# Performance work log

Hardware: AMD Instinct MI355X
Metric: run time of the kernel (lower is better)

## Reference

```python
import jax, jax.numpy as jnp
import numpy as np

N_HEAD = 16
MASK_VALUE = -10000.0


def setup_inputs() -> dict:
    key = jax.random.key(0)
    ks = jax.random.split(key, 5)
    B, S, D = 2, 2048, 1024
    return {
        "x": jax.random.normal(ks[0], (B, S, D), dtype=jnp.float32),
        "qkv_w": jax.random.normal(ks[1], (D, 3 * D), dtype=jnp.float32) * 0.02,
        "qkv_b": jnp.zeros((3 * D,), dtype=jnp.float32),
        "proj_w": jax.random.normal(ks[2], (D, D), dtype=jnp.float32) * 0.02,
        "proj_b": jnp.zeros((D,), dtype=jnp.float32),
    }


def reference(x, qkv_w, qkv_b, proj_w, proj_b):
    B, S, D = x.shape
    H = N_HEAD
    hd = D // H

    # fused QKV projection, then split (torch.split along last dim)
    qkv = x @ qkv_w + qkv_b                      # [B, S, 3D]
    q, k, v = jnp.split(qkv, 3, axis=-1)

    def split_heads(t):  # [B, S, D] -> [B, H, S, hd]
        return t.reshape(B, S, H, hd).transpose(0, 2, 1, 3)

    q, k, v = split_heads(q), split_heads(k), split_heads(v)

    # scaled dot-product scores (scale_attn_weights=True)
    scores = jnp.einsum("bhqd,bhkd->bhqk", q, k) / jnp.sqrt(jnp.asarray(hd, x.dtype))

    # causal mask: tril over [query_len, key_len] (no cache, so q_len == k_len == S)
    causal = jnp.tril(jnp.ones((S, S), dtype=bool))[None, None]
    scores = jnp.where(causal, scores, jnp.asarray(MASK_VALUE, x.dtype))

    attn = jax.nn.softmax(scores, axis=-1)       # dropout p=0 (eval): identity
    out = jnp.einsum("bhqk,bhkd->bhqd", attn, v)

    # merge heads and output projection (resid dropout p=0)
    out = out.transpose(0, 2, 1, 3).reshape(B, S, D)
    out = out @ proj_w + proj_b
    return out
```

## Files before the change

kernel.cpp:

```cpp
#include <hip/hip_runtime.h>
#include <hip/hip_bf16.h>


#define SEQ 2048
#define DM 1024
#define HD 64
#define NHEAD 16
#define BHTOT 32

typedef unsigned short u16;
typedef __bf16 bf16_t;
typedef bf16_t bf16x8 __attribute__((ext_vector_type(8)));
typedef float f32x4 __attribute__((ext_vector_type(4)));
typedef float f32x16 __attribute__((ext_vector_type(16)));

__device__ __forceinline__ u16 f2bf(float f) {
  unsigned u = __float_as_uint(f);
  u += 0x7fffu + ((u >> 16) & 1u);
  return (u16)(u >> 16);
}

__device__ __forceinline__ f32x4 mfma16(uint4 a, uint4 b, f32x4 c) {
  return __builtin_amdgcn_mfma_f32_16x16x32_bf16(
      __builtin_bit_cast(bf16x8, a), __builtin_bit_cast(bf16x8, b), c, 0, 0, 0);
}

__device__ __forceinline__ f32x16 mfma32(uint4 a, uint4 b, f32x16 c) {
  return __builtin_amdgcn_mfma_f32_32x32x16_bf16(
      __builtin_bit_cast(bf16x8, a), __builtin_bit_cast(bf16x8, b), c, 0, 0, 0);
}

__device__ __forceinline__ unsigned cvtpk(float lo, float hi) {
  unsigned d;
  asm("v_cvt_pk_bf16_f32 %0, %1, %2" : "=v"(d) : "v"(lo), "v"(hi));
  return d;
}

__device__ __forceinline__ void gload_lds16(const u16* g, void* l) {
  __builtin_amdgcn_global_load_lds(
      (const __attribute__((address_space(1))) unsigned*)g,
      (__attribute__((address_space(3))) unsigned*)l, 16, 0, 0);
}

__global__ __launch_bounds__(256) void cvt_bf16(const float* __restrict__ in,
                                                u16* __restrict__ out) {
  int i = (blockIdx.x * 256 + threadIdx.x) * 4;
  float4 v = *(const float4*)(in + i);
  uint2 pk;
  pk.x = (unsigned)f2bf(v.x) | ((unsigned)f2bf(v.y) << 16);
  pk.y = (unsigned)f2bf(v.z) | ((unsigned)f2bf(v.w) << 16);
  *(uint2*)(out + i) = pk;
}

__global__ __launch_bounds__(256) void transpose_w(const float* __restrict__ W,
                                                   u16* __restrict__ Wt,
                                                   int K, int N) {
  __shared__ u16 t[32][33];
  const int n0 = blockIdx.x * 32, k0 = blockIdx.y * 32;
  const int tx = threadIdx.x & 31, ty = threadIdx.x >> 5;
#pragma unroll
  for (int i = 0; i < 4; ++i) {
    int k = ty + i * 8;
    t[tx][k] = f2bf(W[(size_t)(k0 + k) * N + n0 + tx]);
  }
  __syncthreads();
#pragma unroll
  for (int i = 0; i < 4; ++i) {
    int n = ty + i * 8;
    Wt[(size_t)(n0 + n) * K + k0 + tx] = t[n][tx];
  }
}

__global__ __launch_bounds__(256) void qkv_gemm(
    const u16* __restrict__ A, const u16* __restrict__ Bt,
    const float* __restrict__ bias,
    u16* __restrict__ qb, u16* __restrict__ kb, u16* __restrict__ vb) {
  __shared__ u16 Al[128 * 32];
  __shared__ u16 Bl[128 * 32];
  const int tid = threadIdx.x;
  const int m0 = blockIdx.y * 128;
  const int n0 = blockIdx.x * 128;
  const int w = tid >> 6, lane = tid & 63;
  const int lr = lane & 15, lg = lane >> 4;
  const int wm = (w >> 1) * 64, wn = (w & 1) * 64;
  const int Kd = DM;

  f32x4 acc[4][4] = {};

  for (int kk = 0; kk < Kd; kk += 32) {
    __syncthreads();
#pragma unroll
    for (int i = 0; i < 2; ++i) {
      int off = (i * 4 + w) * 1024 + lane * 16;
      int row = off >> 6, colb = off & 63;
      gload_lds16(A + (size_t)(m0 + row) * Kd + kk + (colb >> 1),
                  (char*)Al + (i * 4 + w) * 1024);
      gload_lds16(Bt + (size_t)(n0 + row) * Kd + kk + (colb >> 1),
                  (char*)Bl + (i * 4 + w) * 1024);
    }
    __syncthreads();
    uint4 af[4], bfr[4];
#pragma unroll
    for (int mi = 0; mi < 4; ++mi)
      af[mi] = *(const uint4*)(Al + (wm + mi * 16 + lr) * 32 + lg * 8);
#pragma unroll
    for (int ni = 0; ni < 4; ++ni)
      bfr[ni] = *(const uint4*)(Bl + (wn + ni * 16 + lr) * 32 + lg * 8);
#pragma unroll
    for (int mi = 0; mi < 4; ++mi)
#pragma unroll
      for (int ni = 0; ni < 4; ++ni)
        acc[mi][ni] = mfma16(af[mi], bfr[ni], acc[mi][ni]);
  }

#pragma unroll
  for (int mi = 0; mi < 4; ++mi) {
#pragma unroll
    for (int ni = 0; ni < 4; ++ni) {
#pragma unroll
      for (int r = 0; r < 4; ++r) {
        int m = m0 + wm + mi * 16 + lg * 4 + r;
        int n = n0 + wn + ni * 16 + lr;
        float v = acc[mi][ni][r] + bias[n];
        int part = n >> 10;
        int d = n & 1023;
        int h = d >> 6, dim = d & 63;
        int b = m >> 11, s = m & 2047;
        int bh = b * NHEAD + h;
        if (part == 0)
          qb[((size_t)bh * SEQ + s) * HD + dim] = f2bf(v * 0.125f);
        else if (part == 1)
          kb[((size_t)bh * SEQ + s) * HD + dim] = f2bf(v);
        else
          vb[((size_t)bh * HD + dim) * SEQ + s] = f2bf(v);
      }
    }
  }
}

__global__ __launch_bounds__(256) void attn_kernel(
    const u16* __restrict__ Q, const u16* __restrict__ K,
    const u16* __restrict__ Vt, u16* __restrict__ O) {
  const int lane = threadIdx.x & 63;
  const int w = threadIdx.x >> 6;
  const int r31 = lane & 31;
  const int hi = lane >> 5;
  const int bh = blockIdx.x;
  const int y = blockIdx.y;
  const int qt = (w == 0) ? y : (w == 1) ? (31 - y) : (w == 2) ? (32 + y) : (63 - y);
  const int q0w = qt * 32;

  const u16* Qb = Q + (size_t)bh * SEQ * HD;
  const u16* Kb = K + (size_t)bh * SEQ * HD;
  const u16* Vb = Vt + (size_t)bh * HD * SEQ;

  uint4 qf[4];
#pragma unroll
  for (int ks = 0; ks < 4; ++ks)
    qf[ks] = *(const uint4*)(Qb + (size_t)(q0w + r31) * HD + ks * 16 + hi * 8);

  f32x16 ot0 = {}, ot1 = {};
  float M = -1e30f, L = 0.f;

  const int nst = (q0w >> 6) + 1;
  for (int t = 0; t < nst; ++t) {
    const int kv0 = t << 6;
    f32x16 s0 = {}, s1 = {};
#pragma unroll
    for (int ks = 0; ks < 4; ++ks) {
      uint4 kf0 = *(const uint4*)(Kb + (size_t)(kv0 + r31) * HD + ks * 16 + hi * 8);
      uint4 kf1 = *(const uint4*)(Kb + (size_t)(kv0 + 32 + r31) * HD + ks * 16 + hi * 8);
      s0 = mfma32(kf0, qf[ks], s0);
      s1 = mfma32(kf1, qf[ks], s1);
    }
    if (t == nst - 1) {
      const int q_abs = q0w + r31;
#pragma unroll
      for (int i = 0; i < 16; ++i) {
        int row = (i & 3) + 8 * (i >> 2) + 4 * hi;
        if (kv0 + row > q_abs) s0[i] = -1e30f;
        if (kv0 + 32 + row > q_abs) s1[i] = -1e30f;
      }
    }
    float pm = s0[0];
#pragma unroll
    for (int i = 1; i < 16; ++i) pm = fmaxf(pm, s0[i]);
#pragma unroll
    for (int i = 0; i < 16; ++i) pm = fmaxf(pm, s1[i]);
    pm = fmaxf(pm, __shfl_xor(pm, 32));
    const float newM = fmaxf(M, pm);
    const float sc = __expf(M - newM);
    M = newM;
    float rs = 0.f;
#pragma unroll
    for (int i = 0; i < 16; ++i) { s0[i] = __expf(s0[i] - newM); rs += s0[i]; }
#pragma unroll
    for (int i = 0; i < 16; ++i) { s1[i] = __expf(s1[i] - newM); rs += s1[i]; }
    rs += __shfl_xor(rs, 32);
    L = L * sc + rs;
#pragma unroll
    for (int i = 0; i < 16; ++i) { ot0[i] *= sc; ot1[i] *= sc; }

    uint4 pa[4];
#define RELAYOUT(dst, v0, v1, v2, v3, v4, v5, v6, v7)                    \
    {                                                                    \
      unsigned e01 = cvtpk(v0, v1), e23 = cvtpk(v2, v3);                 \
      unsigned e45 = cvtpk(v4, v5), e67 = cvtpk(v6, v7);                 \
      unsigned p01 = __shfl_xor(e01, 32), p23 = __shfl_xor(e23, 32);     \
      unsigned p45 = __shfl_xor(e45, 32), p67 = __shfl_xor(e67, 32);     \
      dst.x = hi ? p45 : e01;                                            \
      dst.y = hi ? p67 : e23;                                            \
      dst.z = hi ? e45 : p01;                                            \
      dst.w = hi ? e67 : p23;                                            \
    }
    RELAYOUT(pa[0], s0[0], s0[1], s0[2], s0[3], s0[4], s0[5], s0[6], s0[7]);
    RELAYOUT(pa[1], s0[8], s0[9], s0[10], s0[11], s0[12], s0[13], s0[14], s0[15]);
    RELAYOUT(pa[2], s1[0], s1[1], s1[2], s1[3], s1[4], s1[5], s1[6], s1[7]);
    RELAYOUT(pa[3], s1[8], s1[9], s1[10], s1[11], s1[12], s1[13], s1[14], s1[15]);
#undef RELAYOUT

#pragma unroll
    for (int ks = 0; ks < 4; ++ks) {
      uint4 vf0 = *(const uint4*)(Vb + (size_t)r31 * SEQ + kv0 + ks * 16 + hi * 8);
      uint4 vf1 = *(const uint4*)(Vb + (size_t)(32 + r31) * SEQ + kv0 + ks * 16 + hi * 8);
      ot0 = mfma32(vf0, pa[ks], ot0);
      ot1 = mfma32(vf1, pa[ks], ot1);
    }
  }

  const float inv = 1.0f / L;
  const int b = bh >> 4, h = bh & 15;
  u16* Orow = O + ((size_t)b * SEQ + q0w + r31) * DM + h * HD;
#pragma unroll
  for (int g = 0; g < 4; ++g) {
    uint2 p0, p1;
    p0.x = (unsigned)f2bf(ot0[4 * g + 0] * inv) | ((unsigned)f2bf(ot0[4 * g + 1] * inv) << 16);
    p0.y = (unsigned)f2bf(ot0[4 * g + 2] * inv) | ((unsigned)f2bf(ot0[4 * g + 3] * inv) << 16);
    p1.x = (unsigned)f2bf(ot1[4 * g + 0] * inv) | ((unsigned)f2bf(ot1[4 * g + 1] * inv) << 16);
    p1.y = (unsigned)f2bf(ot1[4 * g + 2] * inv) | ((unsigned)f2bf(ot1[4 * g + 3] * inv) << 16);
    *(uint2*)(Orow + 8 * g + 4 * hi) = p0;
    *(uint2*)(Orow + 32 + 8 * g + 4 * hi) = p1;
  }
}

__global__ __launch_bounds__(256) void proj_gemm(
    const u16* __restrict__ A, const u16* __restrict__ Bt,
    const float* __restrict__ bias, float* __restrict__ out) {
  __shared__ u16 Al[128 * 32];
  __shared__ u16 Bl[128 * 32];
  const int tid = threadIdx.x;
  const int m0 = blockIdx.y * 128;
  const int n0 = blockIdx.x * 128;
  const int w = tid >> 6, lane = tid & 63;
  const int lr = lane & 15, lg = lane >> 4;
  const int wm = (w >> 1) * 64, wn = (w & 1) * 64;
  const int Kd = DM;

  f32x4 acc[4][4] = {};

  for (int kk = 0; kk < Kd; kk += 32) {
    __syncthreads();
#pragma unroll
    for (int i = 0; i < 2; ++i) {
      int off = (i * 4 + w) * 1024 + lane * 16;
      int row = off >> 6, colb = off & 63;
      gload_lds16(A + (size_t)(m0 + row) * Kd + kk + (colb >> 1),
                  (char*)Al + (i * 4 + w) * 1024);
      gload_lds16(Bt + (size_t)(n0 + row) * Kd + kk + (colb >> 1),
                  (char*)Bl + (i * 4 + w) * 1024);
    }
    __syncthreads();
    uint4 af[4], bfr[4];
#pragma unroll
    for (int mi = 0; mi < 4; ++mi)
      af[mi] = *(const uint4*)(Al + (wm + mi * 16 + lr) * 32 + lg * 8);
#pragma unroll
    for (int ni = 0; ni < 4; ++ni)
      bfr[ni] = *(const uint4*)(Bl + (wn + ni * 16 + lr) * 32 + lg * 8);
#pragma unroll
    for (int mi = 0; mi < 4; ++mi)
#pragma unroll
      for (int ni = 0; ni < 4; ++ni)
        acc[mi][ni] = mfma16(af[mi], bfr[ni], acc[mi][ni]);
  }

#pragma unroll
  for (int mi = 0; mi < 4; ++mi)
#pragma unroll
    for (int ni = 0; ni < 4; ++ni)
#pragma unroll
      for (int r = 0; r < 4; ++r) {
        int m = m0 + wm + mi * 16 + lg * 4 + r;
        int n = n0 + wn + ni * 16 + lr;
        out[(size_t)m * DM + n] = acc[mi][ni][r] + bias[n];
      }
}

extern "C" void kernel_launch(void* const* d_in, const int* in_sizes, int n_in,
                              void* d_out, int out_size, void* d_ws, size_t ws_size,
                              hipStream_t stream) {
  const float* x      = (const float*)d_in[0];
  const float* qkv_w  = (const float*)d_in[1];
  const float* qkv_b  = (const float*)d_in[2];
  const float* proj_w = (const float*)d_in[3];
  const float* proj_b = (const float*)d_in[4];
  float* out = (float*)d_out;

  const size_t per = (size_t)BHTOT * SEQ * HD;
  u16* qb = (u16*)d_ws;
  u16* kb = qb + per;
  u16* vb = kb + per;
  u16* xb = vb + per;
  u16* ab = xb;
  u16* wqkvT = xb + (size_t)SEQ * 2 * DM;
  u16* wprojT = wqkvT + (size_t)DM * 3 * DM / 1;

  wprojT = wqkvT + (size_t)3072 * DM;

  dim3 blk(256);
  cvt_bf16<<<dim3(4096), blk, 0, stream>>>(x, xb);
  transpose_w<<<dim3(96, 32), blk, 0, stream>>>(qkv_w, wqkvT, DM, 3072);
  transpose_w<<<dim3(32, 32), blk, 0, stream>>>(proj_w, wprojT, DM, DM);
  qkv_gemm<<<dim3(24, 32), blk, 0, stream>>>(xb, wqkvT, qkv_b, qb, kb, vb);
  attn_kernel<<<dim3(BHTOT, 16), blk, 0, stream>>>(qb, kb, vb, ab);
  proj_gemm<<<dim3(8, 32), blk, 0, stream>>>(ab, wprojT, proj_b, out);
}
```

Measured before the change: 161.9 us.

## Restructure attention: paired q-tiles per block, K prefetch, exp2, lazy rescale, mask skip

Attention blocks now use 2 waves that handle adjacent 32-row query tiles sharing one KV step range, launched heaviest-first over a 1D grid of 1024 blocks. K tiles are double-buffered in registers so the next step's K load overlaps the current softmax and PV work. Q is prescaled by log2(e)/8 so exp2 can replace exp, and the running max is only rescaled when it grows by more than 8 (lazy rescaling). On the diagonal step, the fully masked half-tile is skipped for even query tiles. The trade-off is more register pressure from the double buffers, and lazy rescaling lets values grow up to 2^8 before renormalising.

Result: faster. 148.0 us (-8.6%).

```diff
diff --git a/kernel.cpp b/kernel.cpp
--- a/kernel.cpp
+++ b/kernel.cpp
@@ -128,7 +128,7 @@
         int b = m >> 11, s = m & 2047;
         int bh = b * NHEAD + h;
         if (part == 0)
-          qb[((size_t)bh * SEQ + s) * HD + dim] = f2bf(v * 0.125f);
+          qb[((size_t)bh * SEQ + s) * HD + dim] = f2bf(v * 0.18033688f);
         else if (part == 1)
           kb[((size_t)bh * SEQ + s) * HD + dim] = f2bf(v);
         else
@@ -138,17 +138,18 @@
   }
 }
 
-__global__ __launch_bounds__(256) void attn_kernel(
+__global__ __launch_bounds__(128) void attn_kernel(
     const u16* __restrict__ Q, const u16* __restrict__ K,
     const u16* __restrict__ Vt, u16* __restrict__ O) {
   const int lane = threadIdx.x & 63;
   const int w = threadIdx.x >> 6;
   const int r31 = lane & 31;
   const int hi = lane >> 5;
-  const int bh = blockIdx.x;
-  const int y = blockIdx.y;
-  const int qt = (w == 0) ? y : (w == 1) ? (31 - y) : (w == 2) ? (32 + y) : (63 - y);
+  const int bh = blockIdx.x & 31;
+  const int j = 31 - (blockIdx.x >> 5);
+  const int qt = 2 * j + w;
   const int q0w = qt * 32;
+  const int nst = j + 1;
 
   const u16* Qb = Q + (size_t)bh * SEQ * HD;
   const u16* Kb = K + (size_t)bh * SEQ * HD;
@@ -162,71 +163,123 @@
   f32x16 ot0 = {}, ot1 = {};
   float M = -1e30f, L = 0.f;
 
-  const int nst = (q0w >> 6) + 1;
-  for (int t = 0; t < nst; ++t) {
-    const int kv0 = t << 6;
-    f32x16 s0 = {}, s1 = {};
-#pragma unroll
-    for (int ks = 0; ks < 4; ++ks) {
-      uint4 kf0 = *(const uint4*)(Kb + (size_t)(kv0 + r31) * HD + ks * 16 + hi * 8);
-      uint4 kf1 = *(const uint4*)(Kb + (size_t)(kv0 + 32 + r31) * HD + ks * 16 + hi * 8);
-      s0 = mfma32(kf0, qf[ks], s0);
-      s1 = mfma32(kf1, qf[ks], s1);
-    }
-    if (t == nst - 1) {
-      const int q_abs = q0w + r31;
-#pragma unroll
-      for (int i = 0; i < 16; ++i) {
-        int row = (i & 3) + 8 * (i >> 2) + 4 * hi;
-        if (kv0 + row > q_abs) s0[i] = -1e30f;
-        if (kv0 + 32 + row > q_abs) s1[i] = -1e30f;
-      }
-    }
-    float pm = s0[0];
-#pragma unroll
-    for (int i = 1; i < 16; ++i) pm = fmaxf(pm, s0[i]);
-#pragma unroll
-    for (int i = 0; i < 16; ++i) pm = fmaxf(pm, s1[i]);
-    pm = fmaxf(pm, __shfl_xor(pm, 32));
-    const float newM = fmaxf(M, pm);
-    const float sc = __expf(M - newM);
-    M = newM;
-    float rs = 0.f;
-#pragma unroll
-    for (int i = 0; i < 16; ++i) { s0[i] = __expf(s0[i] - newM); rs += s0[i]; }
-#pragma unroll
-    for (int i = 0; i < 16; ++i) { s1[i] = __expf(s1[i] - newM); rs += s1[i]; }
-    rs += __shfl_xor(rs, 32);
-    L = L * sc + rs;
-#pragma unroll
-    for (int i = 0; i < 16; ++i) { ot0[i] *= sc; ot1[i] *= sc; }
-
-    uint4 pa[4];
-#define RELAYOUT(dst, v0, v1, v2, v3, v4, v5, v6, v7)                    \
-    {                                                                    \
-      unsigned e01 = cvtpk(v0, v1), e23 = cvtpk(v2, v3);                 \
-      unsigned e45 = cvtpk(v4, v5), e67 = cvtpk(v6, v7);                 \
-      unsigned p01 = __shfl_xor(e01, 32), p23 = __shfl_xor(e23, 32);     \
-      unsigned p45 = __shfl_xor(e45, 32), p67 = __shfl_xor(e67, 32);     \
-      dst.x = hi ? p45 : e01;                                            \
-      dst.y = hi ? p67 : e23;                                            \
-      dst.z = hi ? e45 : p01;                                            \
-      dst.w = hi ? e67 : p23;                                            \
-    }
-    RELAYOUT(pa[0], s0[0], s0[1], s0[2], s0[3], s0[4], s0[5], s0[6], s0[7]);
-    RELAYOUT(pa[1], s0[8], s0[9], s0[10], s0[11], s0[12], s0[13], s0[14], s0[15]);
-    RELAYOUT(pa[2], s1[0], s1[1], s1[2], s1[3], s1[4], s1[5], s1[6], s1[7]);
-    RELAYOUT(pa[3], s1[8], s1[9], s1[10], s1[11], s1[12], s1[13], s1[14], s1[15]);
+#define LOADK(KF, kv0)                                                          \
+  {                                                                             \
+    _Pragma("unroll") for (int ks = 0; ks < 4; ++ks) {                          \
+      KF[ks] = *(const uint4*)(Kb + (size_t)((kv0) + r31) * HD + ks * 16 + hi * 8); \
+      KF[ks + 4] =                                                              \
+          *(const uint4*)(Kb + (size_t)((kv0) + 32 + r31) * HD + ks * 16 + hi * 8); \
+    }                                                                           \
+  }
+
+#define RELAYOUT(dst, S, base)                                                  \
+  {                                                                             \
+    unsigned e01 = cvtpk(S[base + 0], S[base + 1]), e23 = cvtpk(S[base + 2], S[base + 3]); \
+    unsigned e45 = cvtpk(S[base + 4], S[base + 5]), e67 = cvtpk(S[base + 6], S[base + 7]); \
+    unsigned p01 = __shfl_xor(e01, 32), p23 = __shfl_xor(e23, 32);              \
+    unsigned p45 = __shfl_xor(e45, 32), p67 = __shfl_xor(e67, 32);              \
+    dst.x = hi ? p45 : e01;                                                     \
+    dst.y = hi ? p67 : e23;                                                     \
+    dst.z = hi ? e45 : p01;                                                     \
+    dst.w = hi ? e67 : p23;                                                     \
+  }
+
+#define STEP(KF, KN)                                                            \
+  {                                                                             \
+    const int kv0 = t << 6;                                                     \
+    const bool last = (t == nst - 1);                                           \
+    const bool skip1 = last && ((qt & 1) == 0);   \
+    uint4 vf[8];                                                                \
+    _Pragma("unroll") for (int ks = 0; ks < 2; ++ks) {                          \
+      vf[ks] = *(const uint4*)(Vb + (size_t)r31 * SEQ + kv0 + ks * 16 + hi * 8); \
+      vf[ks + 4] =                                                              \
+          *(const uint4*)(Vb + (size_t)(32 + r31) * SEQ + kv0 + ks * 16 + hi * 8); \
+    }                                                                           \
+    if (!skip1) {                                                               \
+      _Pragma("unroll") for (int ks = 2; ks < 4; ++ks) {                        \
+        vf[ks] = *(const uint4*)(Vb + (size_t)r31 * SEQ + kv0 + ks * 16 + hi * 8); \
+        vf[ks + 4] =                                                            \
+            *(const uint4*)(Vb + (size_t)(32 + r31) * SEQ + kv0 + ks * 16 + hi * 8); \
+      }                                                                         \
+    }                                                                           \
+    f32x16 s0 = {}, s1 = {};                                                    \
+    _Pragma("unroll") for (int ks = 0; ks < 4; ++ks)                            \
+        s0 = mfma32(KF[ks], qf[ks], s0);                                        \
+    if (!skip1) {                                                               \
+      _Pragma("unroll") for (int ks = 0; ks < 4; ++ks)                          \
+          s1 = mfma32(KF[ks + 4], qf[ks], s1);                                  \
+    }                                                                           \
+    if (t + 1 < nst) LOADK(KN, kv0 + 64);                                       \
+    if (last) {                                                                 \
+      _Pragma("unroll") for (int i = 0; i < 16; ++i) {                          \
+        const int row = (i & 3) + 8 * (i >> 2) + 4 * hi;                        \
+        if (skip1) {                                                            \
+          if (row > r31) s0[i] = -1e30f;                                        \
+        } else {                                                                \
+          if (row > r31) s1[i] = -1e30f;                                        \
+        }                                                                       \
+      }                                                                         \
+    }                                                                           \
+    float pm = s0[0];                                                           \
+    _Pragma("unroll") for (int i = 1; i < 16; ++i) pm = fmaxf(pm, s0[i]);       \
+    if (!skip1) {                                                               \
+      _Pragma("unroll") for (int i = 0; i < 16; ++i) pm = fmaxf(pm, s1[i]);     \
+    }                                                                           \
+    pm = fmaxf(pm, __shfl_xor(pm, 32));                                         \
+    if (!__all(pm - M <= 8.0f)) {   \
+      const float newM = fmaxf(M, pm);                                          \
+      const float sc = __builtin_exp2f(M - newM);                               \
+      M = newM;                                                                 \
+      L *= sc;                                                                  \
+      _Pragma("unroll") for (int i = 0; i < 16; ++i) {                          \
+        ot0[i] *= sc;                                                           \
+        ot1[i] *= sc;                                                           \
+      }                                                                         \
+    }                                                                           \
+    float rs = 0.f;                                                             \
+    _Pragma("unroll") for (int i = 0; i < 16; ++i) {                            \
+      s0[i] = __builtin_exp2f(s0[i] - M);                                       \
+      rs += s0[i];                                                              \
+    }                                                                           \
+    if (!skip1) {                                                               \
+      _Pragma("unroll") for (int i = 0; i < 16; ++i) {                          \
+        s1[i] = __builtin_exp2f(s1[i] - M);                                     \
+        rs += s1[i];                                                            \
+      }                                                                         \
+    }                                                                           \
+    rs += __shfl_xor(rs, 32);                                                   \
+    L += rs;                                                                    \
+    uint4 pa[4];                                                                \
+    RELAYOUT(pa[0], s0, 0);                                                     \
+    RELAYOUT(pa[1], s0, 8);                                                     \
+    if (!skip1) {                                                               \
+      RELAYOUT(pa[2], s1, 0);                                                   \
+      RELAYOUT(pa[3], s1, 8);                                                   \
+    }                                                                           \
+    _Pragma("unroll") for (int ks = 0; ks < 2; ++ks) {                          \
+      ot0 = mfma32(vf[ks], pa[ks], ot0);                                        \
+      ot1 = mfma32(vf[ks + 4], pa[ks], ot1);                                    \
+    }                                                                           \
+    if (!skip1) {                                                               \
+      _Pragma("unroll") for (int ks = 2; ks < 4; ++ks) {                        \
+        ot0 = mfma32(vf[ks], pa[ks], ot0);                                      \
+        ot1 = mfma32(vf[ks + 4], pa[ks], ot1);                                  \
+      }                                                                         \
+    }                                                                           \
+  }
+
+  uint4 kA[8], kB[8];
+  LOADK(kA, 0);
+  int t = 0;
+  for (;;) {
+    STEP(kA, kB);
+    if (++t >= nst) break;
+    STEP(kB, kA);
+    if (++t >= nst) break;
+  }
+#undef STEP
 #undef RELAYOUT
-
-#pragma unroll
-    for (int ks = 0; ks < 4; ++ks) {
-      uint4 vf0 = *(const uint4*)(Vb + (size_t)r31 * SEQ + kv0 + ks * 16 + hi * 8);
-      uint4 vf1 = *(const uint4*)(Vb + (size_t)(32 + r31) * SEQ + kv0 + ks * 16 + hi * 8);
-      ot0 = mfma32(vf0, pa[ks], ot0);
-      ot1 = mfma32(vf1, pa[ks], ot1);
-    }
-  }
+#undef LOADK
 
   const float inv = 1.0f / L;
   const int b = bh >> 4, h = bh & 15;
@@ -313,15 +366,13 @@
   u16* xb = vb + per;
   u16* ab = xb;
   u16* wqkvT = xb + (size_t)SEQ * 2 * DM;
-  u16* wprojT = wqkvT + (size_t)DM * 3 * DM / 1;
-
-  wprojT = wqkvT + (size_t)3072 * DM;
+  u16* wprojT = wqkvT + (size_t)3072 * DM;
 
   dim3 blk(256);
   cvt_bf16<<<dim3(4096), blk, 0, stream>>>(x, xb);
   transpose_w<<<dim3(96, 32), blk, 0, stream>>>(qkv_w, wqkvT, DM, 3072);
   transpose_w<<<dim3(32, 32), blk, 0, stream>>>(proj_w, wprojT, DM, DM);
   qkv_gemm<<<dim3(24, 32), blk, 0, stream>>>(xb, wqkvT, qkv_b, qb, kb, vb);
-  attn_kernel<<<dim3(BHTOT, 16), blk, 0, stream>>>(qb, kb, vb, ab);
+  attn_kernel<<<dim3(1024), dim3(128), 0, stream>>>(qb, kb, vb, ab);
   proj_gemm<<<dim3(8, 32), blk, 0, stream>>>(ab, wprojT, proj_b, out);
 }
```

## Split attention KV loop across two waves with LDS merge and exp2 softmax

Applied to the files above, without the earlier changes.

Each attention block now handles one 32-row query tile with two waves that split the KV tiles between them (even/odd) and merge their partial softmax states through shared memory. Blocks are ordered longest-first to improve load balance. Q is pre-scaled by log2(e)/8 so exp2 replaces exp, and rescaling of the output is skipped unless the running max grows by more than a threshold. K tiles are prefetched one iteration ahead, and the masked half of the diagonal tile is skipped. This costs an LDS merge and a barrier per block, and the lazy rescale risks overflow if scores jump by more than the threshold.

Measured after the change: 151.5 us. -6.4%, faster.

```diff
diff --git a/kernel.cpp b/kernel.cpp
--- a/kernel.cpp
+++ b/kernel.cpp
@@ -128,7 +128,7 @@
         int b = m >> 11, s = m & 2047;
         int bh = b * NHEAD + h;
         if (part == 0)
-          qb[((size_t)bh * SEQ + s) * HD + dim] = f2bf(v * 0.125f);
+          qb[((size_t)bh * SEQ + s) * HD + dim] = f2bf(v * 0.18033688f);
         else if (part == 1)
           kb[((size_t)bh * SEQ + s) * HD + dim] = f2bf(v);
         else
@@ -138,17 +138,19 @@
   }
 }
 
-__global__ __launch_bounds__(256) void attn_kernel(
+__global__ __launch_bounds__(128) void attn_kernel(
     const u16* __restrict__ Q, const u16* __restrict__ K,
     const u16* __restrict__ Vt, u16* __restrict__ O) {
+  __shared__ float mrgO[32][64];
+  __shared__ float mrgM[64], mrgL[64];
   const int lane = threadIdx.x & 63;
   const int w = threadIdx.x >> 6;
   const int r31 = lane & 31;
   const int hi = lane >> 5;
-  const int bh = blockIdx.x;
-  const int y = blockIdx.y;
-  const int qt = (w == 0) ? y : (w == 1) ? (31 - y) : (w == 2) ? (32 + y) : (63 - y);
+  const int bh = blockIdx.x & 31;
+  const int qt = 63 - (blockIdx.x >> 5);
   const int q0w = qt * 32;
+  const int nst = (qt >> 1) + 1;
 
   const u16* Qb = Q + (size_t)bh * SEQ * HD;
   const u16* Kb = K + (size_t)bh * SEQ * HD;
@@ -162,84 +164,160 @@
   f32x16 ot0 = {}, ot1 = {};
   float M = -1e30f, L = 0.f;
 
-  const int nst = (q0w >> 6) + 1;
-  for (int t = 0; t < nst; ++t) {
+#define LOADK(KF, kv0)                                                          \
+  {                                                                             \
+    _Pragma("unroll") for (int ks = 0; ks < 4; ++ks) {                          \
+      KF[ks] = *(const uint4*)(Kb + (size_t)((kv0) + r31) * HD + ks * 16 + hi * 8); \
+      KF[ks + 4] =                                                              \
+          *(const uint4*)(Kb + (size_t)((kv0) + 32 + r31) * HD + ks * 16 + hi * 8); \
+    }                                                                           \
+  }
+
+#define RELAYOUT(dst, S, base)                                                  \
+  {                                                                             \
+    unsigned e01 = cvtpk(S[base + 0], S[base + 1]), e23 = cvtpk(S[base + 2], S[base + 3]); \
+    unsigned e45 = cvtpk(S[base + 4], S[base + 5]), e67 = cvtpk(S[base + 6], S[base + 7]); \
+    unsigned p01 = __shfl_xor(e01, 32), p23 = __shfl_xor(e23, 32);              \
+    unsigned p45 = __shfl_xor(e45, 32), p67 = __shfl_xor(e67, 32);              \
+    dst.x = hi ? p45 : e01;                                                     \
+    dst.y = hi ? p67 : e23;                                                     \
+    dst.z = hi ? e45 : p01;                                                     \
+    dst.w = hi ? e67 : p23;                                                     \
+  }
+
+  uint4 kA[8];
+  if (w < nst) LOADK(kA, w * 64);
+
+  for (int t = w; t < nst; t += 2) {
     const int kv0 = t << 6;
+    const bool last = (t == nst - 1);
+    const bool skip1 = last && ((qt & 1) == 0);
+    uint4 vf[8];
+#pragma unroll
+    for (int ks = 0; ks < 2; ++ks) {
+      vf[ks] = *(const uint4*)(Vb + (size_t)r31 * SEQ + kv0 + ks * 16 + hi * 8);
+      vf[ks + 4] = *(const uint4*)(Vb + (size_t)(32 + r31) * SEQ + kv0 + ks * 16 + hi * 8);
+    }
+    if (!skip1) {
+#pragma unroll
+      for (int ks = 2; ks < 4; ++ks) {
+        vf[ks] = *(const uint4*)(Vb + (size_t)r31 * SEQ + kv0 + ks * 16 + hi * 8);
+        vf[ks + 4] = *(const uint4*)(Vb + (size_t)(32 + r31) * SEQ + kv0 + ks * 16 + hi * 8);
+      }
+    }
     f32x16 s0 = {}, s1 = {};
 #pragma unroll
-    for (int ks = 0; ks < 4; ++ks) {
-      uint4 kf0 = *(const uint4*)(Kb + (size_t)(kv0 + r31) * HD + ks * 16 + hi * 8);
-      uint4 kf1 = *(const uint4*)(Kb + (size_t)(kv0 + 32 + r31) * HD + ks * 16 + hi * 8);
-      s0 = mfma32(kf0, qf[ks], s0);
-      s1 = mfma32(kf1, qf[ks], s1);
-    }
-    if (t == nst - 1) {
-      const int q_abs = q0w + r31;
+    for (int ks = 0; ks < 4; ++ks) s0 = mfma32(kA[ks], qf[ks], s0);
+    if (!skip1) {
+#pragma unroll
+      for (int ks = 0; ks < 4; ++ks) s1 = mfma32(kA[ks + 4], qf[ks], s1);
+    }
+    if (t + 2 < nst) LOADK(kA, (t + 2) << 6);
+    if (last) {
 #pragma unroll
       for (int i = 0; i < 16; ++i) {
-        int row = (i & 3) + 8 * (i >> 2) + 4 * hi;
-        if (kv0 + row > q_abs) s0[i] = -1e30f;
-        if (kv0 + 32 + row > q_abs) s1[i] = -1e30f;
+        const int row = (i & 3) + 8 * (i >> 2) + 4 * hi;
+        if (skip1) {
+          if (row > r31) s0[i] = -1e30f;
+        } else {
+          if (row > r31) s1[i] = -1e30f;
+        }
       }
     }
     float pm = s0[0];
 #pragma unroll
     for (int i = 1; i < 16; ++i) pm = fmaxf(pm, s0[i]);
-#pragma unroll
-    for (int i = 0; i < 16; ++i) pm = fmaxf(pm, s1[i]);
+    if (!skip1) {
+#pragma unroll
+      for (int i = 0; i < 16; ++i) pm = fmaxf(pm, s1[i]);
+    }
     pm = fmaxf(pm, __shfl_xor(pm, 32));
-    const float newM = fmaxf(M, pm);
-    const float sc = __expf(M - newM);
-    M = newM;
+    if (!__all(pm - M <= 8.0f)) {
+      const float newM = fmaxf(M, pm);
+      const float sc = __builtin_exp2f(M - newM);
+      M = newM;
+      L *= sc;
+#pragma unroll
+      for (int i = 0; i < 16; ++i) {
+        ot0[i] *= sc;
+        ot1[i] *= sc;
+      }
+    }
     float rs = 0.f;
 #pragma unroll
-    for (int i = 0; i < 16; ++i) { s0[i] = __expf(s0[i] - newM); rs += s0[i]; }
-#pragma unroll
-    for (int i = 0; i < 16; ++i) { s1[i] = __expf(s1[i] - newM); rs += s1[i]; }
+    for (int i = 0; i < 16; ++i) {
+      s0[i] = __builtin_exp2f(s0[i] - M);
+      rs += s0[i];
+    }
+    if (!skip1) {
+#pragma unroll
+      for (int i = 0; i < 16; ++i) {
+        s1[i] = __builtin_exp2f(s1[i] - M);
+        rs += s1[i];
+      }
+    }
     rs += __shfl_xor(rs, 32);
-    L = L * sc + rs;
-#pragma unroll
-    for (int i = 0; i < 16; ++i) { ot0[i] *= sc; ot1[i] *= sc; }
-
+    L += rs;
     uint4 pa[4];
-#define RELAYOUT(dst, v0, v1, v2, v3, v4, v5, v6, v7)                    \
-    {                                                                    \
-      unsigned e01 = cvtpk(v0, v1), e23 = cvtpk(v2, v3);                 \
-      unsigned e45 = cvtpk(v4, v5), e67 = cvtpk(v6, v7);                 \
-      unsigned p01 = __shfl_xor(e01, 32), p23 = __shfl_xor(e23, 32);     \
-      unsigned p45 = __shfl_xor(e45, 32), p67 = __shfl_xor(e67, 32);     \
-      dst.x = hi ? p45 : e01;                                            \
-      dst.y = hi ? p67 : e23;                                            \
-      dst.z = hi ? e45 : p01;                                            \
-      dst.w = hi ? e67 : p23;                                            \
-    }
-    RELAYOUT(pa[0], s0[0], s0[1], s0[2], s0[3], s0[4], s0[5], s0[6], s0[7]);
-    RELAYOUT(pa[1], s0[8], s0[9], s0[10], s0[11], s0[12], s0[13], s0[14], s0[15]);
-    RELAYOUT(pa[2], s1[0], s1[1], s1[2], s1[3], s1[4], s1[5], s1[6], s1[7]);
-    RELAYOUT(pa[3], s1[8], s1[9], s1[10], s1[11], s1[12], s1[13], s1[14], s1[15]);
+    RELAYOUT(pa[0], s0, 0);
+    RELAYOUT(pa[1], s0, 8);
+    if (!skip1) {
+      RELAYOUT(pa[2], s1, 0);
+      RELAYOUT(pa[3], s1, 8);
+    }
+#pragma unroll
+    for (int ks = 0; ks < 2; ++ks) {
+      ot0 = mfma32(vf[ks], pa[ks], ot0);
+      ot1 = mfma32(vf[ks + 4], pa[ks], ot1);
+    }
+    if (!skip1) {
+#pragma unroll
+      for (int ks = 2; ks < 4; ++ks) {
+        ot0 = mfma32(vf[ks], pa[ks], ot0);
+        ot1 = mfma32(vf[ks + 4], pa[ks], ot1);
+      }
+    }
+  }
 #undef RELAYOUT
-
-#pragma unroll
-    for (int ks = 0; ks < 4; ++ks) {
-      uint4 vf0 = *(const uint4*)(Vb + (size_t)r31 * SEQ + kv0 + ks * 16 + hi * 8);
-      uint4 vf1 = *(const uint4*)(Vb + (size_t)(32 + r31) * SEQ + kv0 + ks * 16 + hi * 8);
-      ot0 = mfma32(vf0, pa[ks], ot0);
-      ot1 = mfma32(vf1, pa[ks], ot1);
-    }
-  }
-
-  const float inv = 1.0f / L;
-  const int b = bh >> 4, h = bh & 15;
-  u16* Orow = O + ((size_t)b * SEQ + q0w + r31) * DM + h * HD;
-#pragma unroll
-  for (int g = 0; g < 4; ++g) {
-    uint2 p0, p1;
-    p0.x = (unsigned)f2bf(ot0[4 * g + 0] * inv) | ((unsigned)f2bf(ot0[4 * g + 1] * inv) << 16);
-    p0.y = (unsigned)f2bf(ot0[4 * g + 2] * inv) | ((unsigned)f2bf(ot0[4 * g + 3] * inv) << 16);
-    p1.x = (unsigned)f2bf(ot1[4 * g + 0] * inv) | ((unsigned)f2bf(ot1[4 * g + 1] * inv) << 16);
-    p1.y = (unsigned)f2bf(ot1[4 * g + 2] * inv) | ((unsigned)f2bf(ot1[4 * g + 3] * inv) << 16);
-    *(uint2*)(Orow + 8 * g + 4 * hi) = p0;
-    *(uint2*)(Orow + 32 + 8 * g + 4 * hi) = p1;
+#undef LOADK
+
+  if (w == 1) {
+    mrgM[lane] = M;
+    mrgL[lane] = L;
+#pragma unroll
+    for (int i = 0; i < 16; ++i) {
+      mrgO[i][lane] = ot0[i];
+      mrgO[i + 16][lane] = ot1[i];
+    }
+  }
+  __syncthreads();
+  if (w == 0) {
+    const float M1 = mrgM[lane], L1 = mrgL[lane];
+    const float Mm = fmaxf(M, M1);
+    const float f0 = __builtin_exp2f(M - Mm);
+    const float f1 = __builtin_exp2f(M1 - Mm);
+    const float inv = 1.0f / (L * f0 + L1 * f1);
+    const float c0 = f0 * inv, c1 = f1 * inv;
+    const int b = bh >> 4, h = bh & 15;
+    u16* Orow = O + ((size_t)b * SEQ + q0w + r31) * DM + h * HD;
+#pragma unroll
+    for (int g = 0; g < 4; ++g) {
+      uint2 p0, p1;
+      float v0 = ot0[4 * g + 0] * c0 + mrgO[4 * g + 0][lane] * c1;
+      float v1 = ot0[4 * g + 1] * c0 + mrgO[4 * g + 1][lane] * c1;
+      float v2 = ot0[4 * g + 2] * c0 + mrgO[4 * g + 2][lane] * c1;
+      float v3 = ot0[4 * g + 3] * c0 + mrgO[4 * g + 3][lane] * c1;
+      p0.x = (unsigned)f2bf(v0) | ((unsigned)f2bf(v1) << 16);
+      p0.y = (unsigned)f2bf(v2) | ((unsigned)f2bf(v3) << 16);
+      float u0 = ot1[4 * g + 0] * c0 + mrgO[16 + 4 * g + 0][lane] * c1;
+      float u1 = ot1[4 * g + 1] * c0 + mrgO[16 + 4 * g + 1][lane] * c1;
+      float u2 = ot1[4 * g + 2] * c0 + mrgO[16 + 4 * g + 2][lane] * c1;
+      float u3 = ot1[4 * g + 3] * c0 + mrgO[16 + 4 * g + 3][lane] * c1;
+      p1.x = (unsigned)f2bf(u0) | ((unsigned)f2bf(u1) << 16);
+      p1.y = (unsigned)f2bf(u2) | ((unsigned)f2bf(u3) << 16);
+      *(uint2*)(Orow + 8 * g + 4 * hi) = p0;
+      *(uint2*)(Orow + 32 + 8 * g + 4 * hi) = p1;
+    }
   }
 }
 
@@ -313,15 +391,13 @@
   u16* xb = vb + per;
   u16* ab = xb;
   u16* wqkvT = xb + (size_t)SEQ * 2 * DM;
-  u16* wprojT = wqkvT + (size_t)DM * 3 * DM / 1;
-
-  wprojT = wqkvT + (size_t)3072 * DM;
+  u16* wprojT = wqkvT + (size_t)3072 * DM;
 
   dim3 blk(256);
   cvt_bf16<<<dim3(4096), blk, 0, stream>>>(x, xb);
   transpose_w<<<dim3(96, 32), blk, 0, stream>>>(qkv_w, wqkvT, DM, 3072);
   transpose_w<<<dim3(32, 32), blk, 0, stream>>>(proj_w, wprojT, DM, DM);
   qkv_gemm<<<dim3(24, 32), blk, 0, stream>>>(xb, wqkvT, qkv_b, qb, kb, vb);
-  attn_kernel<<<dim3(BHTOT, 16), blk, 0, stream>>>(qb, kb, vb, ab);
+  attn_kernel<<<dim3(2048), dim3(128), 0, stream>>>(qb, kb, vb, ab);
   proj_gemm<<<dim3(8, 32), blk, 0, stream>>>(ab, wprojT, proj_b, out);
 }
```
